# Kernel tuning notes

Measured on AMD Instinct MI355X. Metric: run time of the kernel, lower is better.

The kernel has to match this reference:

```python
import jax, jax.numpy as jnp
import numpy as np

N = 20000      # num nodes (num_words == num_sents, required by residual/linear reuse)
D = 128        # Dw == Ds (original code applies linear_word to both branches)
NE = 640000    # num edges
NEG_SLOPE = 0.2


def gat_conv(x, src, dst, W, a_src, a_dst, bias, num_nodes):
    """PyG GATConv, heads=1, concat=True. Edges are (src -> dst); softmax over
    incoming edges of each dst node."""
    h = x @ W                                   # (N, D_out)
    s_src = h @ a_src                           # (N,) att score per node as source
    s_dst = h @ a_dst                           # (N,) att score per node as target
    e = jax.nn.leaky_relu(s_src[src] + s_dst[dst], NEG_SLOPE)   # (E,)
    # segment softmax over dst
    emax = jax.ops.segment_max(e, dst, num_segments=num_nodes)  # (N,) -inf for empty ok
    ex = jnp.exp(e - emax[dst])                                  # (E,)
    denom = jax.ops.segment_sum(ex, dst, num_segments=num_nodes)
    alpha = ex / (denom[dst] + 1e-16)                            # (E,)
    out = jax.ops.segment_sum(alpha[:, None] * h[src], dst, num_segments=num_nodes)
    return out + bias


def setup_inputs() -> dict:
    key = jax.random.key(0)
    ks = jax.random.split(key, 12)
    Xw = jax.random.normal(ks[0], (N, D), dtype=jnp.float32)
    Xs = jax.random.normal(ks[1], (N, D), dtype=jnp.float32)
    edge_index = jax.random.randint(ks[2], (2, NE), 0, N)
    sc = 0.1
    return {
        "Xw": Xw,
        "Xs": Xs,
        "edge_index": edge_index,
        # gat_sent2word params (in=Ds, out=Dw)
        "W_s2w": jax.random.normal(ks[3], (D, D), dtype=jnp.float32) * sc,
        "a_src_s2w": jax.random.normal(ks[4], (D,), dtype=jnp.float32) * sc,
        "a_dst_s2w": jax.random.normal(ks[5], (D,), dtype=jnp.float32) * sc,
        "b_s2w": jnp.zeros((D,), dtype=jnp.float32),
        # gat_word2sent params (in=Dw, out=Ds)
        "W_w2s": jax.random.normal(ks[6], (D, D), dtype=jnp.float32) * sc,
        "a_src_w2s": jax.random.normal(ks[7], (D,), dtype=jnp.float32) * sc,
        "a_dst_w2s": jax.random.normal(ks[8], (D,), dtype=jnp.float32) * sc,
        "b_w2s": jnp.zeros((D,), dtype=jnp.float32),
        # linear_word (the original forward uses it for BOTH branches)
        "W_lin": jax.random.normal(ks[9], (D, D), dtype=jnp.float32) * sc,
        "b_lin": jnp.zeros((D,), dtype=jnp.float32),
    }


def reference(Xw, Xs, edge_index, W_s2w, a_src_s2w, a_dst_s2w, b_s2w,
              W_w2s, a_src_w2s, a_dst_w2s, b_w2s, W_lin, b_lin):
    num_nodes = Xw.shape[0]
    src, dst = edge_index[0], edge_index[1]
    # sent2word uses E as-is; word2sent uses Erev (flipped pairs)
    temp_word = gat_conv(Xs, src, dst, W_s2w, a_src_s2w, a_dst_s2w, b_s2w, num_nodes)
    temp_sent = gat_conv(Xw, dst, src, W_w2s, a_src_w2s, a_dst_w2s, b_w2s, num_nodes)
    hidden_word_next = (temp_word + Xw) @ W_lin + b_lin
    # NOTE: original code applies linear_word (not linear_sent) here — kept faithfully
    hidden_sent_next = (temp_sent + Xs) @ W_lin + b_lin
    return (hidden_word_next, hidden_sent_next)
```

## Files before the change

kernel.cpp:

```cpp
#include <hip/hip_runtime.h>
#include <hip/hip_bf16.h>
#include <stdint.h>

#define D 128
#define BKT_W 16
#define BKT_SH 4
#define NB_MAX 2048
#define RPB 128
#define CAPMAX 1024
#define EPT 8

typedef __attribute__((ext_vector_type(8))) short bf16x8;
typedef __attribute__((ext_vector_type(4))) float f32x4;

static __device__ __forceinline__ short f2bf(float x) {
    __hip_bfloat16 h = __float2bfloat16(x);
    return *reinterpret_cast<short*>(&h);
}

__global__ __launch_bounds__(256) void pack_w_k(const float* __restrict__ W0,
                                                const float* __restrict__ W1,
                                                const float* __restrict__ W2,
                                                short* __restrict__ P0,
                                                short* __restrict__ P1,
                                                short* __restrict__ P2,
                                                int* __restrict__ bcur, int nb2) {
    if (blockIdx.x == 0) {
        for (int i = threadIdx.x; i < nb2; i += 256) bcur[i] = 0;
    }
    int t = blockIdx.x * 256 + threadIdx.x;
    int m = t >> 11;
    int r = t & 2047;
    const float* W = (m == 0) ? W0 : (m == 1) ? W1 : W2;
    short*       P = (m == 0) ? P0 : (m == 1) ? P1 : P2;
    int lane = r & 63;
    int fr   = r >> 6;
    int kc = fr >> 3, ct = fr & 7;
    int col = ct * 16 + (lane & 15);
    int kb  = kc * 32 + 4 * (lane >> 4);
    short v[8];
#pragma unroll
    for (int e = 0; e < 8; ++e) {
        int k = kb + (e & 3) + 16 * (e >> 2);
        v[e] = f2bf(W[k * D + col]);
    }
    short* dst = P + (size_t)r * 8;
#pragma unroll
    for (int e = 0; e < 8; ++e) dst[e] = v[e];
}

__global__ __launch_bounds__(256) void fat_h_part_k(
    const float* __restrict__ IN0, const float* __restrict__ IN1,
    const short* __restrict__ P0,  const short* __restrict__ P1,
    short* __restrict__ HB0, short* __restrict__ HB1,
    const float* __restrict__ as0, const float* __restrict__ as1,
    const float* __restrict__ ad0, const float* __restrict__ ad1,
    float* __restrict__ ss0, float* __restrict__ ss1,
    float* __restrict__ sd0, float* __restrict__ sd1,
    int nrows, int mg,
    const int* __restrict__ esrc, const int* __restrict__ edst,
    int* __restrict__ bcur_d, int* __restrict__ bcur_s,
    uint32_t* __restrict__ rec_d, uint32_t* __restrict__ rec_s,
    int ne, int cap) {
    __shared__ __align__(16) char smem[RPB * 136 * 2];
    int bid = blockIdx.x;
    int tid = threadIdx.x;

    if (bid < 2 * mg) {
        int yy = (bid >= mg) ? 1 : 0;
        int xb = bid - yy * mg;
        const float* IN = yy ? IN1 : IN0;
        const short* PK = yy ? P1  : P0;
        short*       HB = yy ? HB1 : HB0;
        const float* a_src = yy ? as1 : as0;
        const float* a_dst = yy ? ad1 : ad0;
        float* ss = yy ? ss1 : ss0;
        float* sd = yy ? sd1 : sd0;
        short* As = (short*)smem;

        int row0 = xb * RPB;
        const float4* in4 = (const float4*)IN;
#pragma unroll
        for (int i = 0; i < 16; ++i) {
            int idx = tid + i * 256;
            int row = idx >> 5;
            int q   = idx & 31;
            float4 v = make_float4(0.f, 0.f, 0.f, 0.f);
            int grow = row0 + row;
            if (grow < nrows) v = in4[(size_t)grow * 32 + q];
            int kc = q >> 3, hi = (q >> 2) & 1, g2 = q & 3;
            short4 s4;
            s4.x = f2bf(v.x); s4.y = f2bf(v.y); s4.z = f2bf(v.z); s4.w = f2bf(v.w);
            *(short4*)&As[row * 136 + kc * 32 + g2 * 8 + hi * 4] = s4;
        }
        __syncthreads();

        int lane = tid & 63;
        int wv   = tid >> 6;
        const bf16x8* Wf = (const bf16x8*)PK;
        f32x4 acc[2][8] = {};
#pragma unroll
        for (int kc = 0; kc < 4; ++kc) {
            bf16x8 a0 = *(const bf16x8*)&As[(wv * 32 +      (lane & 15)) * 136 + kc * 32 + (lane >> 4) * 8];
            bf16x8 a1 = *(const bf16x8*)&As[(wv * 32 + 16 + (lane & 15)) * 136 + kc * 32 + (lane >> 4) * 8];
#pragma unroll
            for (int ct = 0; ct < 8; ++ct) {
                bf16x8 b = Wf[(kc * 8 + ct) * 64 + lane];
                acc[0][ct] = __builtin_amdgcn_mfma_f32_16x16x32_bf16(a0, b, acc[0][ct], 0, 0, 0);
                acc[1][ct] = __builtin_amdgcn_mfma_f32_16x16x32_bf16(a1, b, acc[1][ct], 0, 0, 0);
            }
        }

        int cb = lane & 15, rg = lane >> 4;
        float asv[8], adv[8];
#pragma unroll
        for (int ct = 0; ct < 8; ++ct) { asv[ct] = a_src[ct * 16 + cb]; adv[ct] = a_dst[ct * 16 + cb]; }
#pragma unroll
        for (int rt = 0; rt < 2; ++rt) {
            float ssum[4] = {0, 0, 0, 0}, dsum[4] = {0, 0, 0, 0};
#pragma unroll
            for (int ct = 0; ct < 8; ++ct) {
#pragma unroll
                for (int r = 0; r < 4; ++r) {
                    float x = acc[rt][ct][r];
                    int grow = row0 + wv * 32 + rt * 16 + rg * 4 + r;
                    if (grow < nrows) HB[(size_t)grow * D + ct * 16 + cb] = f2bf(x);
                    ssum[r] += x * asv[ct];
                    dsum[r] += x * adv[ct];
                }
            }
#pragma unroll
            for (int off = 1; off < 16; off <<= 1) {
#pragma unroll
                for (int r = 0; r < 4; ++r) {
                    ssum[r] += __shfl_xor(ssum[r], off);
                    dsum[r] += __shfl_xor(dsum[r], off);
                }
            }
            if (cb == 0) {
#pragma unroll
                for (int r = 0; r < 4; ++r) {
                    int grow = row0 + wv * 32 + rt * 16 + rg * 4 + r;
                    if (grow < nrows) { ss[grow] = ssum[r]; sd[grow] = dsum[r]; }
                }
            }
        }
    } else {
        int pid = bid - 2 * mg;
        int* cnt  = (int*)smem;
        int* base = (int*)(smem + 2 * NB_MAX * 4);
        int blockStart = pid * 256 * EPT;
        for (int i = tid; i < 2 * NB_MAX; i += 256) cnt[i] = 0;
        __syncthreads();
        int s[EPT], d[EPT], sl_d[EPT], sl_s[EPT];
#pragma unroll
        for (int e = 0; e < EPT; ++e) {
            int i = blockStart + e * 256 + tid;
            s[e] = -1;
            if (i < ne) {
                s[e] = esrc[i]; d[e] = edst[i];
                sl_d[e] = atomicAdd(&cnt[0 * NB_MAX + (d[e] >> BKT_SH)], 1);
                sl_s[e] = atomicAdd(&cnt[1 * NB_MAX + (s[e] >> BKT_SH)], 1);
            }
        }
        __syncthreads();
        for (int i = tid; i < 2 * NB_MAX; i += 256) {
            int a = i < NB_MAX ? i : i - NB_MAX;
            if (i < NB_MAX) {
                if (cnt[i]) base[i] = atomicAdd(&bcur_d[a], cnt[i]);
            } else {
                if (cnt[i]) base[i] = atomicAdd(&bcur_s[a], cnt[i]);
            }
        }
        __syncthreads();
#pragma unroll
        for (int e = 0; e < EPT; ++e) {
            if (s[e] >= 0) {
                int bd = d[e] >> BKT_SH, bs = s[e] >> BKT_SH;
                int od = base[0 * NB_MAX + bd] + sl_d[e];
                int os = base[1 * NB_MAX + bs] + sl_s[e];
                if (od < cap) rec_d[(size_t)bd * cap + od] = (uint32_t)s[e] | ((uint32_t)(d[e] & (BKT_W - 1)) << 17);
                if (os < cap) rec_s[(size_t)bs * cap + os] = (uint32_t)d[e] | ((uint32_t)(s[e] & (BKT_W - 1)) << 17);
            }
        }
    }
}

__global__ __launch_bounds__(256) void bucket_gat_ep_k(
    const uint32_t* __restrict__ rec_d, const uint32_t* __restrict__ rec_s,
    const int* __restrict__ bcur_d, const int* __restrict__ bcur_s,
    const float* __restrict__ ss1, const float* __restrict__ sd1,
    const float* __restrict__ ss2, const float* __restrict__ sd2,
    const short* __restrict__ hb1, const short* __restrict__ hb2,
    const float* __restrict__ b1,  const float* __restrict__ b2,
    const float* __restrict__ Xw,  const float* __restrict__ Xs,
    const short* __restrict__ wpkL, const float* __restrict__ b_lin,
    float* __restrict__ out, int n, int nb, int cap) {

    __shared__ __align__(16) char smem0[BKT_W * 136 * 2];
    __shared__ uint32_t srec[CAPMAX];
    __shared__ int deg[BKT_W], scn[BKT_W], cur[BKT_W];
    __shared__ float sdl[BKT_W];

    int bid = blockIdx.x;
    int dirv = (bid >= nb) ? 1 : 0;
    int b = bid - dirv * nb;
    const uint32_t* rec  = dirv ? rec_s  : rec_d;
    const int*      bc   = dirv ? bcur_s : bcur_d;
    const float*    ss   = dirv ? ss2 : ss1;
    const float*    sv   = dirv ? sd2 : sd1;
    const short*    hb   = dirv ? hb2 : hb1;
    const float*    bias = dirv ? b2  : b1;
    const float*    resid= dirv ? Xs  : Xw;
    float*          outp = out + (size_t)dirv * n * D;

    uint32_t* lrec = (uint32_t*)smem0;
    short*    T    = (short*)smem0;

    int tid = threadIdx.x;
    int cnt = bc[b]; if (cnt > cap) cnt = cap;
    int base = b * cap;

    if (tid < BKT_W) {
        deg[tid] = 0;
        int node = b * BKT_W + tid;
        sdl[tid] = (node < n) ? sv[node] : 0.f;
    }
    for (int j = tid; j < cnt; j += 256) lrec[j] = rec[base + j];
    __syncthreads();
    for (int j = tid; j < cnt; j += 256) atomicAdd(&deg[lrec[j] >> 17], 1);
    __syncthreads();
    if (tid < BKT_W) scn[tid] = deg[tid];
    __syncthreads();
    for (int off = 1; off < BKT_W; off <<= 1) {
        int t = (tid < BKT_W && tid >= off) ? scn[tid - off] : 0;
        __syncthreads();
        if (tid < BKT_W) scn[tid] += t;
        __syncthreads();
    }
    if (tid < BKT_W) cur[tid] = scn[tid] - deg[tid];
    __syncthreads();
    for (int j = tid; j < cnt; j += 256) {
        uint32_t r = lrec[j];
        int g  = r >> 17;
        int nbb = (int)(r & 0x1FFFFu);
        float e = ss[nbb] + sdl[g];
        e = (e > 0.f) ? e : 0.2f * e;
        float w = __expf(e);
        srec[atomicAdd(&cur[g], 1)] = (((uint32_t)(unsigned short)f2bf(w)) << 16) | (uint32_t)nbb;
    }
    __syncthreads();

    int wv   = tid >> 6;
    int lane = tid & 63;
    int slot = lane >> 4;
    int c    = lane & 15;
#pragma unroll
    for (int h = 0; h < 4; ++h) {
        int g = wv * 4 + h;
        int node = b * BKT_W + g;
        bool valid = (node < n);
        float acc[8] = {0, 0, 0, 0, 0, 0, 0, 0};
        float wsum = 0.f;
        int beg = scn[g] - deg[g];
        int dg  = valid ? deg[g] : 0;
        uint32_t rpre = (lane < dg) ? srec[beg + lane] : 0u;
        int nfull = (dg < 64) ? dg : 64;
        for (int jj = 0; jj < nfull; jj += 16) {
            uint32_t r[4];
#pragma unroll
            for (int u = 0; u < 4; ++u)
                r[u] = (uint32_t)__shfl((int)rpre, jj + 4 * u + slot);
            uint4 hrow[4];
#pragma unroll
            for (int u = 0; u < 4; ++u)
                hrow[u] = *(const uint4*)(hb + (size_t)(r[u] & 0xFFFFu) * D + c * 8);
#pragma unroll
            for (int u = 0; u < 4; ++u) {
                float w = __uint_as_float(r[u] & 0xFFFF0000u);
                wsum += w;
                const uint32_t* pq = (const uint32_t*)&hrow[u];
#pragma unroll
                for (int q = 0; q < 4; ++q) {
                    uint32_t a = pq[q];
                    acc[2 * q]     += w * __uint_as_float(a << 16);
                    acc[2 * q + 1] += w * __uint_as_float(a & 0xFFFF0000u);
                }
            }
        }
        for (int j = 64; j < dg; j += 16) {
            uint32_t r[4];
#pragma unroll
            for (int u = 0; u < 4; ++u) {
                int idx = j + 4 * u + slot;
                r[u] = (idx < dg) ? srec[beg + idx] : 0u;
            }
#pragma unroll
            for (int u = 0; u < 4; ++u) {
                uint4 hrow = *(const uint4*)(hb + (size_t)(r[u] & 0xFFFFu) * D + c * 8);
                float w = __uint_as_float(r[u] & 0xFFFF0000u);
                wsum += w;
                const uint32_t* pq = (const uint32_t*)&hrow;
#pragma unroll
                for (int q = 0; q < 4; ++q) {
                    uint32_t a = pq[q];
                    acc[2 * q]     += w * __uint_as_float(a << 16);
                    acc[2 * q + 1] += w * __uint_as_float(a & 0xFFFF0000u);
                }
            }
        }
#pragma unroll
        for (int off = 16; off <= 32; off <<= 1) {
            wsum += __shfl_xor(wsum, off);
#pragma unroll
            for (int q = 0; q < 8; ++q) acc[q] += __shfl_xor(acc[q], off);
        }
        if (lane < 16) {
            float v[8];
            if (valid) {
                float inv = 1.0f / (wsum + 1e-16f);
                size_t o = (size_t)node * D + lane * 8;
                float4 r0 = *(const float4*)(resid + o);
                float4 r1 = *(const float4*)(resid + o + 4);
                float4 bb0 = *(const float4*)(bias + lane * 8);
                float4 bb1 = *(const float4*)(bias + lane * 8 + 4);
                v[0] = acc[0] * inv + bb0.x + r0.x;
                v[1] = acc[1] * inv + bb0.y + r0.y;
                v[2] = acc[2] * inv + bb0.z + r0.z;
                v[3] = acc[3] * inv + bb0.w + r0.w;
                v[4] = acc[4] * inv + bb1.x + r1.x;
                v[5] = acc[5] * inv + bb1.y + r1.y;
                v[6] = acc[6] * inv + bb1.z + r1.z;
                v[7] = acc[7] * inv + bb1.w + r1.w;
            } else {
#pragma unroll
                for (int m = 0; m < 8; ++m) v[m] = 0.f;
            }
#pragma unroll
            for (int half = 0; half < 2; ++half) {
                int k0 = lane * 8 + half * 4;
                int kc = k0 >> 5, hi = (k0 >> 4) & 1, g2 = (k0 >> 2) & 3;
                short4 s4;
                s4.x = f2bf(v[half * 4 + 0]);
                s4.y = f2bf(v[half * 4 + 1]);
                s4.z = f2bf(v[half * 4 + 2]);
                s4.w = f2bf(v[half * 4 + 3]);
                *(short4*)&T[g * 136 + kc * 32 + g2 * 8 + hi * 4] = s4;
            }
        }
    }
    __syncthreads();

    const bf16x8* Wf = (const bf16x8*)wpkL;
#pragma unroll
    for (int q = 0; q < 2; ++q) {
        int ct = wv * 2 + q;
        f32x4 acc2 = {};
#pragma unroll
        for (int kc = 0; kc < 4; ++kc) {
            bf16x8 a = *(const bf16x8*)&T[(lane & 15) * 136 + kc * 32 + (lane >> 4) * 8];
            bf16x8 bfr = Wf[(kc * 8 + ct) * 64 + lane];
            acc2 = __builtin_amdgcn_mfma_f32_16x16x32_bf16(a, bfr, acc2, 0, 0, 0);
        }
        int cb = lane & 15, rg = lane >> 4;
        float bv = b_lin[ct * 16 + cb];
#pragma unroll
        for (int r = 0; r < 4; ++r) {
            int grow = b * BKT_W + rg * 4 + r;
            if (grow < n) outp[(size_t)grow * D + ct * 16 + cb] = acc2[r] + bv;
        }
    }
}

extern "C" void kernel_launch(void* const* d_in, const int* in_sizes, int n_in,
                              void* d_out, int out_size, void* d_ws, size_t ws_size,
                              hipStream_t stream) {
    const float* Xw    = (const float*)d_in[0];
    const float* Xs    = (const float*)d_in[1];
    const int*   edge  = (const int*)d_in[2];
    const float* W_s2w = (const float*)d_in[3];
    const float* as1   = (const float*)d_in[4];
    const float* ad1   = (const float*)d_in[5];
    const float* b1    = (const float*)d_in[6];
    const float* W_w2s = (const float*)d_in[7];
    const float* as2   = (const float*)d_in[8];
    const float* ad2   = (const float*)d_in[9];
    const float* b2    = (const float*)d_in[10];
    const float* W_lin = (const float*)d_in[11];
    const float* b_lin = (const float*)d_in[12];
    float* out = (float*)d_out;

    const int N  = in_sizes[0] / D;
    const int NE = in_sizes[2] / 2;
    const int NB = (N + BKT_W - 1) / BKT_W;
    int CAP = ((NE / NB) * 3 / 2 + 255) & ~255;
    if (CAP > CAPMAX) CAP = CAPMAX;
    const int* e_src = edge;
    const int* e_dst = edge + NE;

    char* p = (char*)d_ws;
    auto take = [&](size_t bytes) -> void* {
        p = (char*)(((uintptr_t)p + 255) & ~(uintptr_t)255);
        void* r = (void*)p;
        p += bytes;
        return r;
    };
    short* hb1  = (short*)take((size_t)N * D * 2);
    short* hb2  = (short*)take((size_t)N * D * 2);
    short* wpk1 = (short*)take((size_t)D * D * 2);
    short* wpk2 = (short*)take((size_t)D * D * 2);
    short* wpkL = (short*)take((size_t)D * D * 2);
    float* ss1  = (float*)take((size_t)N * 4);
    float* sd1  = (float*)take((size_t)N * 4);
    float* ss2  = (float*)take((size_t)N * 4);
    float* sd2  = (float*)take((size_t)N * 4);
    int*   bcur = (int*)take((size_t)2 * NB * 4);
    int*   bcur_d = bcur;
    int*   bcur_s = bcur + NB;
    uint32_t* rec_d = (uint32_t*)take((size_t)NB * CAP * 4);
    uint32_t* rec_s = (uint32_t*)take((size_t)NB * CAP * 4);

    pack_w_k<<<24, 256, 0, stream>>>(W_s2w, W_w2s, W_lin, wpk1, wpk2, wpkL, bcur, 2 * NB);

    int mg = (N + RPB - 1) / RPB;
    int partGrid = (NE + 256 * EPT - 1) / (256 * EPT);
    fat_h_part_k<<<2 * mg + partGrid, 256, 0, stream>>>(
        Xs, Xw, wpk1, wpk2, hb1, hb2,
        as1, as2, ad1, ad2, ss1, ss2, sd1, sd2, N, mg,
        e_src, e_dst, bcur_d, bcur_s, rec_d, rec_s, NE, CAP);

    bucket_gat_ep_k<<<2 * NB, 256, 0, stream>>>(
        rec_d, rec_s, bcur_d, bcur_s, ss1, sd1, ss2, sd2,
        hb1, hb2, b1, b2, Xw, Xs, wpkL, b_lin, out, N, NB, CAP);
}
```

Baseline: 83.64 us.

## Bucket edges into coarse 128-node bins and filter per fine block

Partitioning now scatters edges into coarse buckets of 128 nodes instead of 16, so the partition blocks touch far fewer global bucket counters. Each fine 16-node consumer block reads its whole coarse bucket into registers and keeps only the records whose sub-bucket bits match its own. This cuts global atomic contention and scattered writes in partitioning. In exchange, each coarse bucket is read eight times, and capacity clamping now happens at coarse granularity.

```diff
diff --git a/kernel.cpp b/kernel.cpp
--- a/kernel.cpp
+++ b/kernel.cpp
@@ -4,10 +4,13 @@
 
 #define D 128
 #define BKT_W 16
-#define BKT_SH 4
-#define NB_MAX 2048
+#define BKT_C 128
+#define BKT_CSH 7
+#define NBC_MAX 256
 #define RPB 128
-#define CAPMAX 1024
+#define CAPC_MAX 8192
+#define CAPF 1024
+#define RSTG 24
 #define EPT 8
 
 typedef __attribute__((ext_vector_type(8))) short bf16x8;
@@ -61,7 +64,7 @@
     const int* __restrict__ esrc, const int* __restrict__ edst,
     int* __restrict__ bcur_d, int* __restrict__ bcur_s,
     uint32_t* __restrict__ rec_d, uint32_t* __restrict__ rec_s,
-    int ne, int cap) {
+    int ne, int capc) {
     __shared__ __align__(16) char smem[RPB * 136 * 2];
     int bid = blockIdx.x;
     int tid = threadIdx.x;
@@ -148,9 +151,9 @@
     } else {
         int pid = bid - 2 * mg;
         int* cnt  = (int*)smem;
-        int* base = (int*)(smem + 2 * NB_MAX * 4);
+        int* base = (int*)(smem + 2 * NBC_MAX * 4);
         int blockStart = pid * 256 * EPT;
-        for (int i = tid; i < 2 * NB_MAX; i += 256) cnt[i] = 0;
+        for (int i = tid; i < 2 * NBC_MAX; i += 256) cnt[i] = 0;
         __syncthreads();
         int s[EPT], d[EPT], sl_d[EPT], sl_s[EPT];
 #pragma unroll
@@ -159,28 +162,25 @@
             s[e] = -1;
             if (i < ne) {
                 s[e] = esrc[i]; d[e] = edst[i];
-                sl_d[e] = atomicAdd(&cnt[0 * NB_MAX + (d[e] >> BKT_SH)], 1);
-                sl_s[e] = atomicAdd(&cnt[1 * NB_MAX + (s[e] >> BKT_SH)], 1);
-            }
-        }
-        __syncthreads();
-        for (int i = tid; i < 2 * NB_MAX; i += 256) {
-            int a = i < NB_MAX ? i : i - NB_MAX;
-            if (i < NB_MAX) {
-                if (cnt[i]) base[i] = atomicAdd(&bcur_d[a], cnt[i]);
-            } else {
-                if (cnt[i]) base[i] = atomicAdd(&bcur_s[a], cnt[i]);
-            }
+                sl_d[e] = atomicAdd(&cnt[0 * NBC_MAX + (d[e] >> BKT_CSH)], 1);
+                sl_s[e] = atomicAdd(&cnt[1 * NBC_MAX + (s[e] >> BKT_CSH)], 1);
+            }
+        }
+        __syncthreads();
+        for (int i = tid; i < 2 * NBC_MAX; i += 256) {
+            int a = (i < NBC_MAX) ? i : i - NBC_MAX;
+            if (cnt[i]) base[i] = (i < NBC_MAX) ? atomicAdd(&bcur_d[a], cnt[i])
+                                                : atomicAdd(&bcur_s[a], cnt[i]);
         }
         __syncthreads();
 #pragma unroll
         for (int e = 0; e < EPT; ++e) {
             if (s[e] >= 0) {
-                int bd = d[e] >> BKT_SH, bs = s[e] >> BKT_SH;
-                int od = base[0 * NB_MAX + bd] + sl_d[e];
-                int os = base[1 * NB_MAX + bs] + sl_s[e];
-                if (od < cap) rec_d[(size_t)bd * cap + od] = (uint32_t)s[e] | ((uint32_t)(d[e] & (BKT_W - 1)) << 17);
-                if (os < cap) rec_s[(size_t)bs * cap + os] = (uint32_t)d[e] | ((uint32_t)(s[e] & (BKT_W - 1)) << 17);
+                int bd = d[e] >> BKT_CSH, bs = s[e] >> BKT_CSH;
+                int od = base[0 * NBC_MAX + bd] + sl_d[e];
+                int os = base[1 * NBC_MAX + bs] + sl_s[e];
+                if (od < capc) rec_d[(size_t)bd * capc + od] = (uint32_t)s[e] | ((uint32_t)(d[e] & (BKT_C - 1)) << 17);
+                if (os < capc) rec_s[(size_t)bs * capc + os] = (uint32_t)d[e] | ((uint32_t)(s[e] & (BKT_C - 1)) << 17);
             }
         }
     }
@@ -195,16 +195,18 @@
     const float* __restrict__ b1,  const float* __restrict__ b2,
     const float* __restrict__ Xw,  const float* __restrict__ Xs,
     const short* __restrict__ wpkL, const float* __restrict__ b_lin,
-    float* __restrict__ out, int n, int nb, int cap) {
-
-    __shared__ __align__(16) char smem0[BKT_W * 136 * 2];
-    __shared__ uint32_t srec[CAPMAX];
+    float* __restrict__ out, int n, int nbf, int capc) {
+
+    __shared__ __align__(16) short T[BKT_W * 136];
+    __shared__ uint32_t srec[CAPF];
     __shared__ int deg[BKT_W], scn[BKT_W], cur[BKT_W];
     __shared__ float sdl[BKT_W];
 
     int bid = blockIdx.x;
-    int dirv = (bid >= nb) ? 1 : 0;
-    int b = bid - dirv * nb;
+    int dirv = (bid >= nbf) ? 1 : 0;
+    int b = bid - dirv * nbf;
+    int cb = b >> 3;
+    int sub = b & 7;
     const uint32_t* rec  = dirv ? rec_s  : rec_d;
     const int*      bc   = dirv ? bcur_s : bcur_d;
     const float*    ss   = dirv ? ss2 : ss1;
@@ -214,21 +216,28 @@
     const float*    resid= dirv ? Xs  : Xw;
     float*          outp = out + (size_t)dirv * n * D;
 
-    uint32_t* lrec = (uint32_t*)smem0;
-    short*    T    = (short*)smem0;
-
     int tid = threadIdx.x;
-    int cnt = bc[b]; if (cnt > cap) cnt = cap;
-    int base = b * cap;
+    int cnt = bc[cb]; if (cnt > capc) cnt = capc;
+    size_t cbase = (size_t)cb * capc;
 
     if (tid < BKT_W) {
         deg[tid] = 0;
         int node = b * BKT_W + tid;
         sdl[tid] = (node < n) ? sv[node] : 0.f;
     }
-    for (int j = tid; j < cnt; j += 256) lrec[j] = rec[base + j];
-    __syncthreads();
-    for (int j = tid; j < cnt; j += 256) atomicAdd(&deg[lrec[j] >> 17], 1);
+    uint32_t rr[RSTG];
+#pragma unroll
+    for (int i = 0; i < RSTG; ++i) {
+        int idx = tid + i * 256;
+        rr[i] = (idx < cnt) ? rec[cbase + idx] : 0u;
+    }
+    __syncthreads();
+#pragma unroll
+    for (int i = 0; i < RSTG; ++i) {
+        int idx = tid + i * 256;
+        if (idx < cnt && (int)((rr[i] >> 21) & 7) == sub)
+            atomicAdd(&deg[(rr[i] >> 17) & 15], 1);
+    }
     __syncthreads();
     if (tid < BKT_W) scn[tid] = deg[tid];
     __syncthreads();
@@ -240,14 +249,18 @@
     }
     if (tid < BKT_W) cur[tid] = scn[tid] - deg[tid];
     __syncthreads();
-    for (int j = tid; j < cnt; j += 256) {
-        uint32_t r = lrec[j];
-        int g  = r >> 17;
-        int nbb = (int)(r & 0x1FFFFu);
-        float e = ss[nbb] + sdl[g];
-        e = (e > 0.f) ? e : 0.2f * e;
-        float w = __expf(e);
-        srec[atomicAdd(&cur[g], 1)] = (((uint32_t)(unsigned short)f2bf(w)) << 16) | (uint32_t)nbb;
+#pragma unroll
+    for (int i = 0; i < RSTG; ++i) {
+        int idx = tid + i * 256;
+        if (idx < cnt && (int)((rr[i] >> 21) & 7) == sub) {
+            int g   = (rr[i] >> 17) & 15;
+            int nbb = (int)(rr[i] & 0x1FFFFu);
+            float e = ss[nbb] + sdl[g];
+            e = (e > 0.f) ? e : 0.2f * e;
+            float w = __expf(e);
+            int pos = atomicAdd(&cur[g], 1);
+            if (pos < CAPF) srec[pos] = (((uint32_t)(unsigned short)f2bf(w)) << 16) | (uint32_t)nbb;
+        }
     }
     __syncthreads();
 
@@ -362,12 +375,12 @@
             bf16x8 bfr = Wf[(kc * 8 + ct) * 64 + lane];
             acc2 = __builtin_amdgcn_mfma_f32_16x16x32_bf16(a, bfr, acc2, 0, 0, 0);
         }
-        int cb = lane & 15, rg = lane >> 4;
-        float bv = b_lin[ct * 16 + cb];
+        int cbv = lane & 15, rg = lane >> 4;
+        float bv = b_lin[ct * 16 + cbv];
 #pragma unroll
         for (int r = 0; r < 4; ++r) {
             int grow = b * BKT_W + rg * 4 + r;
-            if (grow < n) outp[(size_t)grow * D + ct * 16 + cb] = acc2[r] + bv;
+            if (grow < n) outp[(size_t)grow * D + ct * 16 + cbv] = acc2[r] + bv;
         }
     }
 }
@@ -392,9 +405,11 @@
 
     const int N  = in_sizes[0] / D;
     const int NE = in_sizes[2] / 2;
-    const int NB = (N + BKT_W - 1) / BKT_W;
-    int CAP = ((NE / NB) * 3 / 2 + 255) & ~255;
-    if (CAP > CAPMAX) CAP = CAPMAX;
+    const int NBC = (N + BKT_C - 1) / BKT_C;
+    const int NBF = (N + BKT_W - 1) / BKT_W;
+    int CAPC = ((NE / NBC) * 3 / 2 + 255) & ~255;
+    if (CAPC > CAPC_MAX) CAPC = CAPC_MAX;
+    if (CAPC > RSTG * 256) CAPC = RSTG * 256;
     const int* e_src = edge;
     const int* e_dst = edge + NE;
 
@@ -414,22 +429,22 @@
     float* sd1  = (float*)take((size_t)N * 4);
     float* ss2  = (float*)take((size_t)N * 4);
     float* sd2  = (float*)take((size_t)N * 4);
-    int*   bcur = (int*)take((size_t)2 * NB * 4);
+    int*   bcur = (int*)take((size_t)2 * NBC * 4);
     int*   bcur_d = bcur;
-    int*   bcur_s = bcur + NB;
-    uint32_t* rec_d = (uint32_t*)take((size_t)NB * CAP * 4);
-    uint32_t* rec_s = (uint32_t*)take((size_t)NB * CAP * 4);
-
-    pack_w_k<<<24, 256, 0, stream>>>(W_s2w, W_w2s, W_lin, wpk1, wpk2, wpkL, bcur, 2 * NB);
+    int*   bcur_s = bcur + NBC;
+    uint32_t* rec_d = (uint32_t*)take((size_t)NBC * CAPC * 4);
+    uint32_t* rec_s = (uint32_t*)take((size_t)NBC * CAPC * 4);
+
+    pack_w_k<<<24, 256, 0, stream>>>(W_s2w, W_w2s, W_lin, wpk1, wpk2, wpkL, bcur, 2 * NBC);
 
     int mg = (N + RPB - 1) / RPB;
     int partGrid = (NE + 256 * EPT - 1) / (256 * EPT);
     fat_h_part_k<<<2 * mg + partGrid, 256, 0, stream>>>(
         Xs, Xw, wpk1, wpk2, hb1, hb2,
         as1, as2, ad1, ad2, ss1, ss2, sd1, sd2, N, mg,
-        e_src, e_dst, bcur_d, bcur_s, rec_d, rec_s, NE, CAP);
-
-    bucket_gat_ep_k<<<2 * NB, 256, 0, stream>>>(
+        e_src, e_dst, bcur_d, bcur_s, rec_d, rec_s, NE, CAPC);
+
+    bucket_gat_ep_k<<<2 * NBF, 256, 0, stream>>>(
         rec_d, rec_s, bcur_d, bcur_s, ss1, sd1, ss2, sd2,
-        hb1, hb2, b1, b2, Xw, Xs, wpkL, b_lin, out, N, NB, CAP);
+        hb1, hb2, b1, b2, Xw, Xs, wpkL, b_lin, out, N, NBF, CAPC);
 }
```

After: 85.45 us. 1.02x slower.

## Split bf16 H into two 64-column halves and gather each half separately

Applied to the files above, without the earlier changes.

The bf16 projected features H are now stored as two separate N×64 arrays, one per column half, instead of one N×128 array. The aggregation kernel makes two passes over each node's incoming edges, one per half, so each gathered row segment is 128 bytes. This keeps each half's working set smaller for cache reuse during the random gathers. In exchange, the edge records are shuffled and read twice, the weight sum is carried between passes through shared memory, and lrec gets its own shared buffer instead of aliasing T, which raises LDS use per block.

```diff
diff --git a/kernel.cpp b/kernel.cpp
--- a/kernel.cpp
+++ b/kernel.cpp
@@ -52,7 +52,8 @@
 __global__ __launch_bounds__(256) void fat_h_part_k(
     const float* __restrict__ IN0, const float* __restrict__ IN1,
     const short* __restrict__ P0,  const short* __restrict__ P1,
-    short* __restrict__ HB0, short* __restrict__ HB1,
+    short* __restrict__ HB0a, short* __restrict__ HB0b,
+    short* __restrict__ HB1a, short* __restrict__ HB1b,
     const float* __restrict__ as0, const float* __restrict__ as1,
     const float* __restrict__ ad0, const float* __restrict__ ad1,
     float* __restrict__ ss0, float* __restrict__ ss1,
@@ -71,7 +72,8 @@
         int xb = bid - yy * mg;
         const float* IN = yy ? IN1 : IN0;
         const short* PK = yy ? P1  : P0;
-        short*       HB = yy ? HB1 : HB0;
+        short*       HBa = yy ? HB1a : HB0a;
+        short*       HBb = yy ? HB1b : HB0b;
         const float* a_src = yy ? as1 : as0;
         const float* a_dst = yy ? ad1 : ad0;
         float* ss = yy ? ss1 : ss0;
@@ -120,11 +122,13 @@
             float ssum[4] = {0, 0, 0, 0}, dsum[4] = {0, 0, 0, 0};
 #pragma unroll
             for (int ct = 0; ct < 8; ++ct) {
+                short* hbt = (ct < 4) ? HBa : HBb;
+                int colh = (ct & 3) * 16 + cb;
 #pragma unroll
                 for (int r = 0; r < 4; ++r) {
                     float x = acc[rt][ct][r];
                     int grow = row0 + wv * 32 + rt * 16 + rg * 4 + r;
-                    if (grow < nrows) HB[(size_t)grow * D + ct * 16 + cb] = f2bf(x);
+                    if (grow < nrows) hbt[(size_t)grow * 64 + colh] = f2bf(x);
                     ssum[r] += x * asv[ct];
                     dsum[r] += x * adv[ct];
                 }
@@ -191,16 +195,19 @@
     const int* __restrict__ bcur_d, const int* __restrict__ bcur_s,
     const float* __restrict__ ss1, const float* __restrict__ sd1,
     const float* __restrict__ ss2, const float* __restrict__ sd2,
-    const short* __restrict__ hb1, const short* __restrict__ hb2,
+    const short* __restrict__ hb1a, const short* __restrict__ hb1b,
+    const short* __restrict__ hb2a, const short* __restrict__ hb2b,
     const float* __restrict__ b1,  const float* __restrict__ b2,
     const float* __restrict__ Xw,  const float* __restrict__ Xs,
     const short* __restrict__ wpkL, const float* __restrict__ b_lin,
     float* __restrict__ out, int n, int nb, int cap) {
 
-    __shared__ __align__(16) char smem0[BKT_W * 136 * 2];
+    __shared__ __align__(16) short T[BKT_W * 136];
     __shared__ uint32_t srec[CAPMAX];
+    __shared__ uint32_t lrec[CAPMAX];
     __shared__ int deg[BKT_W], scn[BKT_W], cur[BKT_W];
     __shared__ float sdl[BKT_W];
+    __shared__ float sinv[BKT_W];
 
     int bid = blockIdx.x;
     int dirv = (bid >= nb) ? 1 : 0;
@@ -209,17 +216,15 @@
     const int*      bc   = dirv ? bcur_s : bcur_d;
     const float*    ss   = dirv ? ss2 : ss1;
     const float*    sv   = dirv ? sd2 : sd1;
-    const short*    hb   = dirv ? hb2 : hb1;
+    const short*    hbA  = dirv ? hb2a : hb1a;
+    const short*    hbB  = dirv ? hb2b : hb1b;
     const float*    bias = dirv ? b2  : b1;
     const float*    resid= dirv ? Xs  : Xw;
     float*          outp = out + (size_t)dirv * n * D;
 
-    uint32_t* lrec = (uint32_t*)smem0;
-    short*    T    = (short*)smem0;
-
     int tid = threadIdx.x;
     int cnt = bc[b]; if (cnt > cap) cnt = cap;
-    int base = b * cap;
+    size_t base = (size_t)b * cap;
 
     if (tid < BKT_W) {
         deg[tid] = 0;
@@ -251,101 +256,110 @@
     }
     __syncthreads();
 
-    int wv   = tid >> 6;
-    int lane = tid & 63;
-    int slot = lane >> 4;
-    int c    = lane & 15;
-#pragma unroll
-    for (int h = 0; h < 4; ++h) {
-        int g = wv * 4 + h;
-        int node = b * BKT_W + g;
-        bool valid = (node < n);
-        float acc[8] = {0, 0, 0, 0, 0, 0, 0, 0};
-        float wsum = 0.f;
-        int beg = scn[g] - deg[g];
-        int dg  = valid ? deg[g] : 0;
-        uint32_t rpre = (lane < dg) ? srec[beg + lane] : 0u;
-        int nfull = (dg < 64) ? dg : 64;
-        for (int jj = 0; jj < nfull; jj += 16) {
-            uint32_t r[4];
-#pragma unroll
-            for (int u = 0; u < 4; ++u)
-                r[u] = (uint32_t)__shfl((int)rpre, jj + 4 * u + slot);
-            uint4 hrow[4];
-#pragma unroll
-            for (int u = 0; u < 4; ++u)
-                hrow[u] = *(const uint4*)(hb + (size_t)(r[u] & 0xFFFFu) * D + c * 8);
-#pragma unroll
-            for (int u = 0; u < 4; ++u) {
-                float w = __uint_as_float(r[u] & 0xFFFF0000u);
-                wsum += w;
-                const uint32_t* pq = (const uint32_t*)&hrow[u];
+    int wv    = tid >> 6;
+    int lane  = tid & 63;
+    int slot8 = lane >> 3;
+    int c8    = lane & 7;
+#pragma unroll
+    for (int half = 0; half < 2; ++half) {
+        const short* hbh = half ? hbB : hbA;
+#pragma unroll
+        for (int h = 0; h < 4; ++h) {
+            int g = wv * 4 + h;
+            int node = b * BKT_W + g;
+            bool valid = (node < n);
+            float acc[8] = {0, 0, 0, 0, 0, 0, 0, 0};
+            float wsum = 0.f;
+            int beg = scn[g] - deg[g];
+            int dg  = valid ? deg[g] : 0;
+            uint32_t rpre = (lane < dg) ? srec[beg + lane] : 0u;
+            int nfull = (dg < 64) ? dg : 64;
+            for (int jj = 0; jj < nfull; jj += 16) {
+                uint32_t r0 = (uint32_t)__shfl((int)rpre, jj + slot8);
+                uint32_t r1 = (uint32_t)__shfl((int)rpre, jj + 8 + slot8);
+                uint4 h0 = *(const uint4*)(hbh + (size_t)(r0 & 0xFFFFu) * 64 + c8 * 8);
+                uint4 h1 = *(const uint4*)(hbh + (size_t)(r1 & 0xFFFFu) * 64 + c8 * 8);
+                float w0 = __uint_as_float(r0 & 0xFFFF0000u);
+                float w1 = __uint_as_float(r1 & 0xFFFF0000u);
+                if (half == 0) wsum += w0 + w1;
+                const uint32_t* p0 = (const uint32_t*)&h0;
+                const uint32_t* p1 = (const uint32_t*)&h1;
 #pragma unroll
                 for (int q = 0; q < 4; ++q) {
-                    uint32_t a = pq[q];
-                    acc[2 * q]     += w * __uint_as_float(a << 16);
-                    acc[2 * q + 1] += w * __uint_as_float(a & 0xFFFF0000u);
-                }
-            }
-        }
-        for (int j = 64; j < dg; j += 16) {
-            uint32_t r[4];
-#pragma unroll
-            for (int u = 0; u < 4; ++u) {
-                int idx = j + 4 * u + slot;
-                r[u] = (idx < dg) ? srec[beg + idx] : 0u;
-            }
-#pragma unroll
-            for (int u = 0; u < 4; ++u) {
-                uint4 hrow = *(const uint4*)(hb + (size_t)(r[u] & 0xFFFFu) * D + c * 8);
-                float w = __uint_as_float(r[u] & 0xFFFF0000u);
-                wsum += w;
-                const uint32_t* pq = (const uint32_t*)&hrow;
+                    uint32_t a = p0[q];
+                    acc[2 * q]     += w0 * __uint_as_float(a << 16);
+                    acc[2 * q + 1] += w0 * __uint_as_float(a & 0xFFFF0000u);
+                    uint32_t bb = p1[q];
+                    acc[2 * q]     += w1 * __uint_as_float(bb << 16);
+                    acc[2 * q + 1] += w1 * __uint_as_float(bb & 0xFFFF0000u);
+                }
+            }
+            for (int j = 64; j < dg; j += 16) {
+                int i0 = j + slot8, i1 = j + 8 + slot8;
+                uint32_t r0 = (i0 < dg) ? srec[beg + i0] : 0u;
+                uint32_t r1 = (i1 < dg) ? srec[beg + i1] : 0u;
+                uint4 h0 = *(const uint4*)(hbh + (size_t)(r0 & 0xFFFFu) * 64 + c8 * 8);
+                uint4 h1 = *(const uint4*)(hbh + (size_t)(r1 & 0xFFFFu) * 64 + c8 * 8);
+                float w0 = __uint_as_float(r0 & 0xFFFF0000u);
+                float w1 = __uint_as_float(r1 & 0xFFFF0000u);
+                if (half == 0) wsum += w0 + w1;
+                const uint32_t* p0 = (const uint32_t*)&h0;
+                const uint32_t* p1 = (const uint32_t*)&h1;
 #pragma unroll
                 for (int q = 0; q < 4; ++q) {
-                    uint32_t a = pq[q];
-                    acc[2 * q]     += w * __uint_as_float(a << 16);
-                    acc[2 * q + 1] += w * __uint_as_float(a & 0xFFFF0000u);
-                }
-            }
-        }
-#pragma unroll
-        for (int off = 16; off <= 32; off <<= 1) {
-            wsum += __shfl_xor(wsum, off);
-#pragma unroll
-            for (int q = 0; q < 8; ++q) acc[q] += __shfl_xor(acc[q], off);
-        }
-        if (lane < 16) {
-            float v[8];
-            if (valid) {
-                float inv = 1.0f / (wsum + 1e-16f);
-                size_t o = (size_t)node * D + lane * 8;
-                float4 r0 = *(const float4*)(resid + o);
-                float4 r1 = *(const float4*)(resid + o + 4);
-                float4 bb0 = *(const float4*)(bias + lane * 8);
-                float4 bb1 = *(const float4*)(bias + lane * 8 + 4);
-                v[0] = acc[0] * inv + bb0.x + r0.x;
-                v[1] = acc[1] * inv + bb0.y + r0.y;
-                v[2] = acc[2] * inv + bb0.z + r0.z;
-                v[3] = acc[3] * inv + bb0.w + r0.w;
-                v[4] = acc[4] * inv + bb1.x + r1.x;
-                v[5] = acc[5] * inv + bb1.y + r1.y;
-                v[6] = acc[6] * inv + bb1.z + r1.z;
-                v[7] = acc[7] * inv + bb1.w + r1.w;
+                    uint32_t a = p0[q];
+                    acc[2 * q]     += w0 * __uint_as_float(a << 16);
+                    acc[2 * q + 1] += w0 * __uint_as_float(a & 0xFFFF0000u);
+                    uint32_t bb = p1[q];
+                    acc[2 * q]     += w1 * __uint_as_float(bb << 16);
+                    acc[2 * q + 1] += w1 * __uint_as_float(bb & 0xFFFF0000u);
+                }
+            }
+#pragma unroll
+            for (int off = 8; off <= 32; off <<= 1) {
+                if (half == 0) wsum += __shfl_xor(wsum, off);
+#pragma unroll
+                for (int q = 0; q < 8; ++q) acc[q] += __shfl_xor(acc[q], off);
+            }
+            float inv;
+            if (half == 0) {
+                inv = 1.0f / (wsum + 1e-16f);
+                if (lane == 0) sinv[g] = inv;
             } else {
-#pragma unroll
-                for (int m = 0; m < 8; ++m) v[m] = 0.f;
-            }
-#pragma unroll
-            for (int half = 0; half < 2; ++half) {
-                int k0 = lane * 8 + half * 4;
-                int kc = k0 >> 5, hi = (k0 >> 4) & 1, g2 = (k0 >> 2) & 3;
-                short4 s4;
-                s4.x = f2bf(v[half * 4 + 0]);
-                s4.y = f2bf(v[half * 4 + 1]);
-                s4.z = f2bf(v[half * 4 + 2]);
-                s4.w = f2bf(v[half * 4 + 3]);
-                *(short4*)&T[g * 136 + kc * 32 + g2 * 8 + hi * 4] = s4;
+                inv = sinv[g];
+            }
+            if (lane < 8) {
+                int col0 = half * 64 + lane * 8;
+                float v[8];
+                if (valid) {
+                    size_t o = (size_t)node * D + col0;
+                    float4 r0v = *(const float4*)(resid + o);
+                    float4 r1v = *(const float4*)(resid + o + 4);
+                    float4 bb0 = *(const float4*)(bias + col0);
+                    float4 bb1 = *(const float4*)(bias + col0 + 4);
+                    v[0] = acc[0] * inv + bb0.x + r0v.x;
+                    v[1] = acc[1] * inv + bb0.y + r0v.y;
+                    v[2] = acc[2] * inv + bb0.z + r0v.z;
+                    v[3] = acc[3] * inv + bb0.w + r0v.w;
+                    v[4] = acc[4] * inv + bb1.x + r1v.x;
+                    v[5] = acc[5] * inv + bb1.y + r1v.y;
+                    v[6] = acc[6] * inv + bb1.z + r1v.z;
+                    v[7] = acc[7] * inv + bb1.w + r1v.w;
+                } else {
+#pragma unroll
+                    for (int m = 0; m < 8; ++m) v[m] = 0.f;
+                }
+#pragma unroll
+                for (int q4 = 0; q4 < 2; ++q4) {
+                    int k0 = col0 + q4 * 4;
+                    int kc = k0 >> 5, hi = (k0 >> 4) & 1, g2 = (k0 >> 2) & 3;
+                    short4 s4;
+                    s4.x = f2bf(v[q4 * 4 + 0]);
+                    s4.y = f2bf(v[q4 * 4 + 1]);
+                    s4.z = f2bf(v[q4 * 4 + 2]);
+                    s4.w = f2bf(v[q4 * 4 + 3]);
+                    *(short4*)&T[g * 136 + kc * 32 + g2 * 8 + hi * 4] = s4;
+                }
             }
         }
     }
@@ -362,12 +376,12 @@
             bf16x8 bfr = Wf[(kc * 8 + ct) * 64 + lane];
             acc2 = __builtin_amdgcn_mfma_f32_16x16x32_bf16(a, bfr, acc2, 0, 0, 0);
         }
-        int cb = lane & 15, rg = lane >> 4;
-        float bv = b_lin[ct * 16 + cb];
+        int cbv = lane & 15, rg = lane >> 4;
+        float bv = b_lin[ct * 16 + cbv];
 #pragma unroll
         for (int r = 0; r < 4; ++r) {
             int grow = b * BKT_W + rg * 4 + r;
-            if (grow < n) outp[(size_t)grow * D + ct * 16 + cb] = acc2[r] + bv;
+            if (grow < n) outp[(size_t)grow * D + ct * 16 + cbv] = acc2[r] + bv;
         }
     }
 }
@@ -405,8 +419,10 @@
         p += bytes;
         return r;
     };
-    short* hb1  = (short*)take((size_t)N * D * 2);
-    short* hb2  = (short*)take((size_t)N * D * 2);
+    short* hb1a = (short*)take((size_t)N * 64 * 2);
+    short* hb1b = (short*)take((size_t)N * 64 * 2);
+    short* hb2a = (short*)take((size_t)N * 64 * 2);
+    short* hb2b = (short*)take((size_t)N * 64 * 2);
     short* wpk1 = (short*)take((size_t)D * D * 2);
     short* wpk2 = (short*)take((size_t)D * D * 2);
     short* wpkL = (short*)take((size_t)D * D * 2);
@@ -425,11 +441,11 @@
     int mg = (N + RPB - 1) / RPB;
     int partGrid = (NE + 256 * EPT - 1) / (256 * EPT);
     fat_h_part_k<<<2 * mg + partGrid, 256, 0, stream>>>(
-        Xs, Xw, wpk1, wpk2, hb1, hb2,
+        Xs, Xw, wpk1, wpk2, hb1a, hb1b, hb2a, hb2b,
         as1, as2, ad1, ad2, ss1, ss2, sd1, sd2, N, mg,
         e_src, e_dst, bcur_d, bcur_s, rec_d, rec_s, NE, CAP);
 
     bucket_gat_ep_k<<<2 * NB, 256, 0, stream>>>(
         rec_d, rec_s, bcur_d, bcur_s, ss1, sd1, ss2, sd2,
-        hb1, hb2, b1, b2, Xw, Xs, wpkL, b_lin, out, N, NB, CAP);
+        hb1a, hb1b, hb2a, hb2b, b1, b2, Xw, Xs, wpkL, b_lin, out, N, NB, CAP);
 }
```

New measurement: 97.59 us. +16.7%, slower.

## Rework edge partitioning to two-pass count/scatter with more edges per block

Applied to the files above, without the earlier changes.

Edge partition blocks now handle 32 edge groups per thread instead of 8. A first pass only counts bucket occupancy, and a second pass re-reads the edges and claims slots with shared atomics on the base offsets, instead of keeping per-edge slots in registers. This cuts the number of partition blocks and the global atomics on bucket cursors, at the cost of reading the edge list twice and serialising the scatter on LDS atomics. The gather kernel unrolls the neighbor loop 8-wide for more loads in flight, and gives lrec its own shared buffer rather than aliasing it with T.

```diff
diff --git a/kernel.cpp b/kernel.cpp
--- a/kernel.cpp
+++ b/kernel.cpp
@@ -8,7 +8,7 @@
 #define NB_MAX 2048
 #define RPB 128
 #define CAPMAX 1024
-#define EPT 8
+#define EPT2 32
 
 typedef __attribute__((ext_vector_type(8))) short bf16x8;
 typedef __attribute__((ext_vector_type(4))) float f32x4;
@@ -149,38 +149,33 @@
         int pid = bid - 2 * mg;
         int* cnt  = (int*)smem;
         int* base = (int*)(smem + 2 * NB_MAX * 4);
-        int blockStart = pid * 256 * EPT;
+        int blockStart = pid * 256 * EPT2;
         for (int i = tid; i < 2 * NB_MAX; i += 256) cnt[i] = 0;
         __syncthreads();
-        int s[EPT], d[EPT], sl_d[EPT], sl_s[EPT];
-#pragma unroll
-        for (int e = 0; e < EPT; ++e) {
+        for (int e = 0; e < EPT2; ++e) {
             int i = blockStart + e * 256 + tid;
-            s[e] = -1;
             if (i < ne) {
-                s[e] = esrc[i]; d[e] = edst[i];
-                sl_d[e] = atomicAdd(&cnt[0 * NB_MAX + (d[e] >> BKT_SH)], 1);
-                sl_s[e] = atomicAdd(&cnt[1 * NB_MAX + (s[e] >> BKT_SH)], 1);
+                atomicAdd(&cnt[0 * NB_MAX + (edst[i] >> BKT_SH)], 1);
+                atomicAdd(&cnt[1 * NB_MAX + (esrc[i] >> BKT_SH)], 1);
             }
         }
         __syncthreads();
         for (int i = tid; i < 2 * NB_MAX; i += 256) {
-            int a = i < NB_MAX ? i : i - NB_MAX;
-            if (i < NB_MAX) {
-                if (cnt[i]) base[i] = atomicAdd(&bcur_d[a], cnt[i]);
-            } else {
-                if (cnt[i]) base[i] = atomicAdd(&bcur_s[a], cnt[i]);
-            }
-        }
-        __syncthreads();
-#pragma unroll
-        for (int e = 0; e < EPT; ++e) {
-            if (s[e] >= 0) {
-                int bd = d[e] >> BKT_SH, bs = s[e] >> BKT_SH;
-                int od = base[0 * NB_MAX + bd] + sl_d[e];
-                int os = base[1 * NB_MAX + bs] + sl_s[e];
-                if (od < cap) rec_d[(size_t)bd * cap + od] = (uint32_t)s[e] | ((uint32_t)(d[e] & (BKT_W - 1)) << 17);
-                if (os < cap) rec_s[(size_t)bs * cap + os] = (uint32_t)d[e] | ((uint32_t)(s[e] & (BKT_W - 1)) << 17);
+            int a = (i < NB_MAX) ? i : i - NB_MAX;
+            int cv = cnt[i];
+            base[i] = cv ? ((i < NB_MAX) ? atomicAdd(&bcur_d[a], cv)
+                                         : atomicAdd(&bcur_s[a], cv)) : 0;
+        }
+        __syncthreads();
+        for (int e = 0; e < EPT2; ++e) {
+            int i = blockStart + e * 256 + tid;
+            if (i < ne) {
+                int s = esrc[i], d = edst[i];
+                int bd = d >> BKT_SH, bs = s >> BKT_SH;
+                int od = atomicAdd(&base[0 * NB_MAX + bd], 1);
+                int os = atomicAdd(&base[1 * NB_MAX + bs], 1);
+                if (od < cap) rec_d[(size_t)bd * cap + od] = (uint32_t)s | ((uint32_t)(d & (BKT_W - 1)) << 17);
+                if (os < cap) rec_s[(size_t)bs * cap + os] = (uint32_t)d | ((uint32_t)(s & (BKT_W - 1)) << 17);
             }
         }
     }
@@ -197,8 +192,9 @@
     const short* __restrict__ wpkL, const float* __restrict__ b_lin,
     float* __restrict__ out, int n, int nb, int cap) {
 
-    __shared__ __align__(16) char smem0[BKT_W * 136 * 2];
+    __shared__ __align__(16) short T[BKT_W * 136];
     __shared__ uint32_t srec[CAPMAX];
+    __shared__ uint32_t lrec[CAPMAX];
     __shared__ int deg[BKT_W], scn[BKT_W], cur[BKT_W];
     __shared__ float sdl[BKT_W];
 
@@ -214,12 +210,9 @@
     const float*    resid= dirv ? Xs  : Xw;
     float*          outp = out + (size_t)dirv * n * D;
 
-    uint32_t* lrec = (uint32_t*)smem0;
-    short*    T    = (short*)smem0;
-
     int tid = threadIdx.x;
     int cnt = bc[b]; if (cnt > cap) cnt = cap;
-    int base = b * cap;
+    size_t base = (size_t)b * cap;
 
     if (tid < BKT_W) {
         deg[tid] = 0;
@@ -266,17 +259,17 @@
         int dg  = valid ? deg[g] : 0;
         uint32_t rpre = (lane < dg) ? srec[beg + lane] : 0u;
         int nfull = (dg < 64) ? dg : 64;
-        for (int jj = 0; jj < nfull; jj += 16) {
-            uint32_t r[4];
-#pragma unroll
-            for (int u = 0; u < 4; ++u)
+        for (int jj = 0; jj < nfull; jj += 32) {
+            uint32_t r[8];
+#pragma unroll
+            for (int u = 0; u < 8; ++u)
                 r[u] = (uint32_t)__shfl((int)rpre, jj + 4 * u + slot);
-            uint4 hrow[4];
-#pragma unroll
-            for (int u = 0; u < 4; ++u)
+            uint4 hrow[8];
+#pragma unroll
+            for (int u = 0; u < 8; ++u)
                 hrow[u] = *(const uint4*)(hb + (size_t)(r[u] & 0xFFFFu) * D + c * 8);
 #pragma unroll
-            for (int u = 0; u < 4; ++u) {
+            for (int u = 0; u < 8; ++u) {
                 float w = __uint_as_float(r[u] & 0xFFFF0000u);
                 wsum += w;
                 const uint32_t* pq = (const uint32_t*)&hrow[u];
@@ -362,12 +355,12 @@
             bf16x8 bfr = Wf[(kc * 8 + ct) * 64 + lane];
             acc2 = __builtin_amdgcn_mfma_f32_16x16x32_bf16(a, bfr, acc2, 0, 0, 0);
         }
-        int cb = lane & 15, rg = lane >> 4;
-        float bv = b_lin[ct * 16 + cb];
+        int cbv = lane & 15, rg = lane >> 4;
+        float bv = b_lin[ct * 16 + cbv];
 #pragma unroll
         for (int r = 0; r < 4; ++r) {
             int grow = b * BKT_W + rg * 4 + r;
-            if (grow < n) outp[(size_t)grow * D + ct * 16 + cb] = acc2[r] + bv;
+            if (grow < n) outp[(size_t)grow * D + ct * 16 + cbv] = acc2[r] + bv;
         }
     }
 }
@@ -423,7 +416,7 @@
     pack_w_k<<<24, 256, 0, stream>>>(W_s2w, W_w2s, W_lin, wpk1, wpk2, wpkL, bcur, 2 * NB);
 
     int mg = (N + RPB - 1) / RPB;
-    int partGrid = (NE + 256 * EPT - 1) / (256 * EPT);
+    int partGrid = (NE + 256 * EPT2 - 1) / (256 * EPT2);
     fat_h_part_k<<<2 * mg + partGrid, 256, 0, stream>>>(
         Xs, Xw, wpk1, wpk2, hb1, hb2,
         as1, as2, ad1, ad2, ss1, ss2, sd1, sd2, N, mg,
```

New measurement: 102.3 us. 22.3% more time.
